# Performance work log

Hardware: AMD Instinct MI355X
Metric: run time of the kernel (lower is better)

The kernel has to match this reference:

```python
import jax, jax.numpy as jnp
import numpy as np

N_NODES = 50000
N_GRAPHS = 50
MAX_NODES = 1000  # equal-size graphs
C_IN = 128
C_OUT = 128
N_EDGES = 800000
N_LAYERS = 3
BN_EPS = 1e-5


def setup_inputs() -> dict:
    key = jax.random.key(0)
    ks = jax.random.split(key, 20)
    x = jax.random.normal(ks[0], (N_NODES, C_IN), dtype=jnp.float32)
    edge_index = jax.random.randint(ks[1], (2, N_EDGES), 0, N_NODES, dtype=jnp.int64)
    batch = jnp.repeat(jnp.arange(N_GRAPHS, dtype=jnp.int64), MAX_NODES)
    s_in = 1.0 / np.sqrt(C_IN)
    s_out = 1.0 / np.sqrt(C_OUT)
    fh_W = jax.random.normal(ks[2], (C_IN, C_OUT), dtype=jnp.float32) * s_in
    fh_b = jnp.zeros((C_OUT,), dtype=jnp.float32)
    W1 = jax.random.normal(ks[3], (N_LAYERS, C_OUT, C_OUT), dtype=jnp.float32) * s_out
    b1 = jnp.zeros((N_LAYERS, C_OUT), dtype=jnp.float32)
    g1 = jnp.ones((N_LAYERS, C_OUT), dtype=jnp.float32)
    be1 = jnp.zeros((N_LAYERS, C_OUT), dtype=jnp.float32)
    W2 = jax.random.normal(ks[4], (N_LAYERS, C_OUT, C_OUT), dtype=jnp.float32) * s_out
    b2 = jnp.zeros((N_LAYERS, C_OUT), dtype=jnp.float32)
    g2 = jnp.ones((N_LAYERS, C_OUT), dtype=jnp.float32)
    be2 = jnp.zeros((N_LAYERS, C_OUT), dtype=jnp.float32)
    return {"x": x, "edge_index": edge_index, "batch": batch,
            "fh_W": fh_W, "fh_b": fh_b,
            "W1": W1, "b1": b1, "g1": g1, "be1": be1,
            "W2": W2, "b2": b2, "g2": g2, "be2": be2}


def _bn(h, gamma, beta):
    # training-mode BatchNorm1d over the node dim (biased variance, like torch)
    mu = jnp.mean(h, axis=0)
    var = jnp.var(h, axis=0)
    return (h - mu) * jax.lax.rsqrt(var + BN_EPS) * gamma + beta


def _mlp(h, W1, b1, g1, be1, W2, b2, g2, be2):
    h = jax.nn.relu(_bn(h @ W1 + b1, g1, be1))
    h = jax.nn.relu(_bn(h @ W2 + b2, g2, be2))
    return h


def _to_dense_batch(h, batch):
    # counts per graph -> exclusive starts -> intra-graph position
    ones = jnp.ones((h.shape[0],), dtype=jnp.int32)
    counts = jax.ops.segment_sum(ones, batch, num_segments=N_GRAPHS)
    starts = jnp.cumsum(counts) - counts
    pos = jnp.arange(h.shape[0], dtype=jnp.int32) - starts[batch]
    dense = jnp.zeros((N_GRAPHS, MAX_NODES, h.shape[1]), dtype=h.dtype)
    return dense.at[batch, pos].set(h)


def reference(x, edge_index, batch, fh_W, fh_b, W1, b1, g1, be1, W2, b2, g2, be2):
    src, dst = edge_index[0], edge_index[1]
    h = x @ fh_W + fh_b  # first_head Linear
    outs = [_to_dense_batch(h, batch)]
    for l in range(N_LAYERS):
        # GINConv: mlp((1+eps)*x + sum_{j->i} x_j), eps=0
        agg = jax.ops.segment_sum(h[src], dst, num_segments=N_NODES)
        h = _mlp(h + agg, W1[l], b1[l], g1[l], be1[l], W2[l], b2[l], g2[l], be2[l])
        outs.append(_to_dense_batch(h, batch))
    return jnp.stack(outs)  # [N_LAYERS+1, B, MAX_NODES, C]
```

## Files before the change

### kernel.cpp

```cpp
#include <hip/hip_runtime.h>

#define NN 50000
#define NE 800000
#define CC 128
#define SLAB (NN * CC)
#define BN_EPS 1e-5f

typedef __attribute__((ext_vector_type(8))) short bf16x8;
typedef __attribute__((ext_vector_type(4))) float f32x4;
typedef unsigned short ushort_t;

__device__ inline ushort_t f2bf(float v) {
  unsigned u = __builtin_bit_cast(unsigned, v);
  unsigned r = u + 0x7FFFu + ((u >> 16) & 1u);
  return (ushort_t)(r >> 16);
}

__global__ void zero_int_kernel(int* __restrict__ p, int n) {
  int i = blockIdx.x * blockDim.x + threadIdx.x;
  if (i < n) p[i] = 0;
}

__global__ void count_kernel(const int* __restrict__ dst, int* __restrict__ counts) {
  int e = blockIdx.x * blockDim.x + threadIdx.x;
  if (e < NE) atomicAdd(&counts[dst[e]], 1);
}

__global__ void scan1_kernel(const int* __restrict__ counts, int* __restrict__ excl,
                             int* __restrict__ blocksum) {
  __shared__ int s[256];
  int t = threadIdx.x;
  int i = blockIdx.x * 256 + t;
  int v = (i < NN) ? counts[i] : 0;
  s[t] = v;
  for (int off = 1; off < 256; off <<= 1) {
    __syncthreads();
    int add = (t >= off) ? s[t - off] : 0;
    __syncthreads();
    s[t] += add;
  }
  __syncthreads();
  if (i < NN) excl[i] = s[t] - v;
  if (t == 255) blocksum[blockIdx.x] = s[255];
}

__global__ void scan2_kernel(int* __restrict__ blocksum, int nb) {
  __shared__ int s[256];
  int t = threadIdx.x;
  int v = (t < nb) ? blocksum[t] : 0;
  s[t] = v;
  for (int off = 1; off < 256; off <<= 1) {
    __syncthreads();
    int add = (t >= off) ? s[t - off] : 0;
    __syncthreads();
    s[t] += add;
  }
  __syncthreads();
  if (t < nb) blocksum[t] = s[t] - v;
}

__global__ void scan3_kernel(int* __restrict__ excl, const int* __restrict__ blocksum) {
  int i = blockIdx.x * 256 + threadIdx.x;
  if (i < NN) excl[i] += blocksum[blockIdx.x];
}

__global__ void fill_kernel(const int* __restrict__ src, const int* __restrict__ dst,
                            const int* __restrict__ starts, int* __restrict__ fill,
                            int* __restrict__ bucket) {
  int e = blockIdx.x * blockDim.x + threadIdx.x;
  if (e < NE) {
    int d = dst[e];
    int pos = atomicAdd(&fill[d], 1);
    bucket[starts[d] + pos] = src[e];
  }
}

__global__ void prep_w_kernel(const float* __restrict__ fh_W, const float* __restrict__ W1,
                              const float* __restrict__ W2, short* __restrict__ whi,
                              short* __restrict__ wlo) {
  int m = blockIdx.x;
  const float* src = (m == 0) ? fh_W : ((m <= 3) ? W1 + (m - 1) * CC * CC : W2 + (m - 4) * CC * CC);
  short* hi = whi + m * CC * CC;
  short* lo = wlo + m * CC * CC;
  for (int it = 0; it < 64; ++it) {
    int idx = it * 256 + threadIdx.x;
    int j = idx & 7;
    int l = (idx >> 3) & 63;
    int nt = (idx >> 9) & 7;
    int ks = idx >> 12;
    int n = nt * 16 + (l & 15);
    int k = ks * 32 + ((l >> 4) << 3) + j;
    float v = src[k * CC + n];
    unsigned u = __builtin_bit_cast(unsigned, v);
    unsigned short h = (unsigned short)(u >> 16);
    float hf = __builtin_bit_cast(float, ((unsigned)h) << 16);
    float r = v - hf;
    unsigned ur = __builtin_bit_cast(unsigned, r);
    hi[idx] = (short)h;
    lo[idx] = (short)(ur >> 16);
  }
}

__global__ void gather_kernel(const ushort_t* __restrict__ h16, const int* __restrict__ starts,
                              const int* __restrict__ counts, const int* __restrict__ bucket,
                              float* __restrict__ agg, float* __restrict__ stats) {
  if (blockIdx.x == 0) {
    stats[threadIdx.x] = 0.f;
    stats[256 + threadIdx.x] = 0.f;
  }
  const int node = blockIdx.x * 4 + (threadIdx.x >> 6);
  const int l = threadIdx.x & 63;
  const int j16 = l & 15;
  const int q = l >> 4;
  const uint4* tbl = (const uint4*)h16;

  float acc[8];
  if (q == 0) {
    uint4 u = tbl[node * 16 + j16];
    acc[0] = __builtin_bit_cast(float, u.x << 16);
    acc[1] = __builtin_bit_cast(float, u.x & 0xFFFF0000u);
    acc[2] = __builtin_bit_cast(float, u.y << 16);
    acc[3] = __builtin_bit_cast(float, u.y & 0xFFFF0000u);
    acc[4] = __builtin_bit_cast(float, u.z << 16);
    acc[5] = __builtin_bit_cast(float, u.z & 0xFFFF0000u);
    acc[6] = __builtin_bit_cast(float, u.w << 16);
    acc[7] = __builtin_bit_cast(float, u.w & 0xFFFF0000u);
  } else {
#pragma unroll
    for (int k = 0; k < 8; ++k) acc[k] = 0.f;
  }

  const int s = starts[node];
  const int n = counts[node];
  for (int base = 0; base < n; base += 64) {
    int nb = min(n - base, 64);
    int idx = (l < nb) ? bucket[s + base + l] : 0;
    int jj = 0;
    for (; jj + 8 <= nb; jj += 8) {
      int sr0 = __shfl(idx, jj + q);
      int sr1 = __shfl(idx, jj + 4 + q);
      uint4 a = tbl[sr0 * 16 + j16];
      uint4 b = tbl[sr1 * 16 + j16];
      acc[0] += __builtin_bit_cast(float, a.x << 16);
      acc[1] += __builtin_bit_cast(float, a.x & 0xFFFF0000u);
      acc[2] += __builtin_bit_cast(float, a.y << 16);
      acc[3] += __builtin_bit_cast(float, a.y & 0xFFFF0000u);
      acc[4] += __builtin_bit_cast(float, a.z << 16);
      acc[5] += __builtin_bit_cast(float, a.z & 0xFFFF0000u);
      acc[6] += __builtin_bit_cast(float, a.w << 16);
      acc[7] += __builtin_bit_cast(float, a.w & 0xFFFF0000u);
      acc[0] += __builtin_bit_cast(float, b.x << 16);
      acc[1] += __builtin_bit_cast(float, b.x & 0xFFFF0000u);
      acc[2] += __builtin_bit_cast(float, b.y << 16);
      acc[3] += __builtin_bit_cast(float, b.y & 0xFFFF0000u);
      acc[4] += __builtin_bit_cast(float, b.z << 16);
      acc[5] += __builtin_bit_cast(float, b.z & 0xFFFF0000u);
      acc[6] += __builtin_bit_cast(float, b.w << 16);
      acc[7] += __builtin_bit_cast(float, b.w & 0xFFFF0000u);
    }
    for (; jj < nb; jj += 4) {
      int i = jj + q;
      int sr = __shfl(idx, i);
      if (i < nb) {
        uint4 a = tbl[sr * 16 + j16];
        acc[0] += __builtin_bit_cast(float, a.x << 16);
        acc[1] += __builtin_bit_cast(float, a.x & 0xFFFF0000u);
        acc[2] += __builtin_bit_cast(float, a.y << 16);
        acc[3] += __builtin_bit_cast(float, a.y & 0xFFFF0000u);
        acc[4] += __builtin_bit_cast(float, a.z << 16);
        acc[5] += __builtin_bit_cast(float, a.z & 0xFFFF0000u);
        acc[6] += __builtin_bit_cast(float, a.w << 16);
        acc[7] += __builtin_bit_cast(float, a.w & 0xFFFF0000u);
      }
    }
  }
#pragma unroll
  for (int k = 0; k < 8; ++k) {
    acc[k] += __shfl_xor(acc[k], 16);
    acc[k] += __shfl_xor(acc[k], 32);
  }
  if (q == 0) {
    float4 w0 = make_float4(acc[0], acc[1], acc[2], acc[3]);
    float4 w1 = make_float4(acc[4], acc[5], acc[6], acc[7]);
    *(float4*)&agg[node * CC + j16 * 8] = w0;
    *(float4*)&agg[node * CC + j16 * 8 + 4] = w1;
  }
}

template <bool FUSE_BN, bool STATS, bool W16>
__global__ __launch_bounds__(256) void gemm_mfma_kernel(
    const float* A, const short* __restrict__ Wp_hi, const short* __restrict__ Wp_lo,
    const float* __restrict__ bias, float* out, ushort_t* __restrict__ h16,
    const float* __restrict__ bn_a, const float* __restrict__ bn_d, float* __restrict__ stats) {
  __shared__ float As[64 * 132];
  __shared__ float sred[2 * CC];
  const int t = threadIdx.x;
  const int l = t & 63;
  const int wv = t >> 6;
  const int m0 = blockIdx.x * 64 + wv * 16;
  const int rowbase = blockIdx.x * 64;
  if (STATS) sred[t] = 0.f;

#pragma unroll
  for (int i = 0; i < 8; ++i) {
    int f = i * 256 + t;
    int r = f >> 5;
    int c = (f & 31) * 4;
    int rg = rowbase + r;
    float4 v = make_float4(0.f, 0.f, 0.f, 0.f);
    if (rg < NN) v = *(const float4*)&A[rg * CC + c];
    if (FUSE_BN) {
      v.x = fmaxf(fmaf(v.x, bn_a[c + 0], bn_d[c + 0]), 0.f);
      v.y = fmaxf(fmaf(v.y, bn_a[c + 1], bn_d[c + 1]), 0.f);
      v.z = fmaxf(fmaf(v.z, bn_a[c + 2], bn_d[c + 2]), 0.f);
      v.w = fmaxf(fmaf(v.w, bn_a[c + 3], bn_d[c + 3]), 0.f);
    }
    *(float4*)&As[r * 132 + c] = v;
  }
  __syncthreads();

  f32x4 acc[8];
#pragma unroll
  for (int i = 0; i < 8; ++i) acc[i] = (f32x4){0.f, 0.f, 0.f, 0.f};

  const int arow = (wv * 16 + (l & 15)) * 132;
  const int kg = (l >> 4) * 8;

#pragma unroll
  for (int ks = 0; ks < 4; ++ks) {
    const float* ap = &As[arow + ks * 32 + kg];
    bf16x8 ah, al;
#pragma unroll
    for (int i = 0; i < 8; ++i) {
      float a = ap[i];
      unsigned u = __builtin_bit_cast(unsigned, a);
      unsigned short hbits = (unsigned short)(u >> 16);
      float hf = __builtin_bit_cast(float, ((unsigned)hbits) << 16);
      float r = a - hf;
      unsigned ur = __builtin_bit_cast(unsigned, r);
      ah[i] = (short)hbits;
      al[i] = (short)(ur >> 16);
    }
#pragma unroll
    for (int nt = 0; nt < 8; ++nt) {
      const int base = (ks * 8 + nt) * 512 + l * 8;
      bf16x8 wh = *(const bf16x8*)&Wp_hi[base];
      bf16x8 wl = *(const bf16x8*)&Wp_lo[base];
      acc[nt] = __builtin_amdgcn_mfma_f32_16x16x32_bf16(ah, wh, acc[nt], 0, 0, 0);
      acc[nt] = __builtin_amdgcn_mfma_f32_16x16x32_bf16(al, wh, acc[nt], 0, 0, 0);
      acc[nt] = __builtin_amdgcn_mfma_f32_16x16x32_bf16(ah, wl, acc[nt], 0, 0, 0);
    }
  }

  const int rbase = m0 + (l >> 4) * 4;
  const int cn = l & 15;
#pragma unroll
  for (int nt = 0; nt < 8; ++nt) {
    int c = nt * 16 + cn;
    float bv = bias[c];
    float s = 0.f, qq = 0.f;
#pragma unroll
    for (int r = 0; r < 4; ++r) {
      int rr = rbase + r;
      if (rr < NN) {
        float v = acc[nt][r] + bv;
        out[rr * CC + c] = v;
        if (W16) h16[rr * CC + c] = f2bf(v);
        if (STATS) { s += v; qq += v * v; }
      }
    }
    if (STATS) {
      s += __shfl_xor(s, 16); s += __shfl_xor(s, 32);
      qq += __shfl_xor(qq, 16); qq += __shfl_xor(qq, 32);
      if ((l >> 4) == 0) {
        atomicAdd(&sred[c], s);
        atomicAdd(&sred[CC + c], qq);
      }
    }
  }
  if (STATS) {
    __syncthreads();
    atomicAdd(&stats[t], sred[t]);
  }
}

__global__ void finalize_kernel(const float* __restrict__ stats, const float* __restrict__ g,
                                const float* __restrict__ be, float* __restrict__ bn_a,
                                float* __restrict__ bn_d) {
  int c = threadIdx.x;
  float mu = stats[c] * (1.0f / NN);
  float var = stats[CC + c] * (1.0f / NN) - mu * mu;
  var = fmaxf(var, 0.f);
  float inv = rsqrtf(var + BN_EPS);
  float a = g[c] * inv;
  bn_a[c] = a;
  bn_d[c] = fmaf(-mu, a, be[c]);
}

__global__ void apply_kernel(const float* __restrict__ tmp, const float* __restrict__ bn_a,
                             const float* __restrict__ bn_d, float* __restrict__ outslab,
                             ushort_t* __restrict__ h16) {
  int i = blockIdx.x * blockDim.x + threadIdx.x;
  float4 v = ((const float4*)tmp)[i];
  int c = (i & 31) << 2;
  float4 a = *(const float4*)&bn_a[c];
  float4 d = *(const float4*)&bn_d[c];
  v.x = fmaxf(fmaf(v.x, a.x, d.x), 0.f);
  v.y = fmaxf(fmaf(v.y, a.y, d.y), 0.f);
  v.z = fmaxf(fmaf(v.z, a.z, d.z), 0.f);
  v.w = fmaxf(fmaf(v.w, a.w, d.w), 0.f);
  ((float4*)outslab)[i] = v;
  if (h16) {
    ushort_t p[4] = {f2bf(v.x), f2bf(v.y), f2bf(v.z), f2bf(v.w)};
    *(uint2*)&h16[i * 4] = *(uint2*)p;
  }
}

extern "C" void kernel_launch(void* const* d_in, const int* in_sizes, int n_in,
                              void* d_out, int out_size, void* d_ws, size_t ws_size,
                              hipStream_t stream) {
  const float* x    = (const float*)d_in[0];
  const int*   edge = (const int*)d_in[1];
  const float* fh_W = (const float*)d_in[3];
  const float* fh_b = (const float*)d_in[4];
  const float* W1   = (const float*)d_in[5];
  const float* b1   = (const float*)d_in[6];
  const float* g1   = (const float*)d_in[7];
  const float* be1  = (const float*)d_in[8];
  const float* W2   = (const float*)d_in[9];
  const float* b2   = (const float*)d_in[10];
  const float* g2   = (const float*)d_in[11];
  const float* be2  = (const float*)d_in[12];
  float* out = (float*)d_out;

  const int* src = edge;
  const int* dst = edge + NE;

  int* counts   = (int*)d_ws;
  int* fill     = counts + 50048;
  int* starts   = fill + 50048;
  int* blocksum = starts + 50048;
  int* bucket   = blocksum + 256;
  float* stats  = (float*)(bucket + NE);
  float* bn_a1  = stats + 512;
  float* bn_d1  = bn_a1 + CC;
  float* bn_a2  = bn_d1 + CC;
  float* bn_d2  = bn_a2 + CC;
  short* whi    = (short*)(bn_d2 + CC);
  short* wlo    = whi + 7 * CC * CC;
  ushort_t* h16 = (ushort_t*)(wlo + 7 * CC * CC);
  float* aggbuf = (float*)(h16 + SLAB);

  zero_int_kernel<<<(100096 + 255) / 256, 256, 0, stream>>>(counts, 100096);
  count_kernel<<<NE / 256, 256, 0, stream>>>(dst, counts);
  scan1_kernel<<<196, 256, 0, stream>>>(counts, starts, blocksum);
  scan2_kernel<<<1, 256, 0, stream>>>(blocksum, 196);
  scan3_kernel<<<196, 256, 0, stream>>>(starts, blocksum);
  fill_kernel<<<NE / 256, 256, 0, stream>>>(src, dst, starts, fill, bucket);

  prep_w_kernel<<<7, 256, 0, stream>>>(fh_W, W1, W2, whi, wlo);

  gemm_mfma_kernel<false, false, true><<<782, 256, 0, stream>>>(
      x, whi, wlo, fh_b, out, h16, nullptr, nullptr, nullptr);

  for (int ly = 0; ly < 3; ++ly) {
    gather_kernel<<<NN / 4, 256, 0, stream>>>(h16, starts, counts, bucket, aggbuf, stats);
    gemm_mfma_kernel<false, true, false><<<782, 256, 0, stream>>>(
        aggbuf, whi + (1 + ly) * CC * CC, wlo + (1 + ly) * CC * CC, b1 + ly * CC,
        aggbuf, nullptr, nullptr, nullptr, stats);
    finalize_kernel<<<1, 128, 0, stream>>>(stats, g1 + ly * CC, be1 + ly * CC, bn_a1, bn_d1);
    gemm_mfma_kernel<true, true, false><<<782, 256, 0, stream>>>(
        aggbuf, whi + (4 + ly) * CC * CC, wlo + (4 + ly) * CC * CC, b2 + ly * CC,
        aggbuf, nullptr, bn_a1, bn_d1, stats + 256);
    finalize_kernel<<<1, 128, 0, stream>>>(stats + 256, g2 + ly * CC, be2 + ly * CC, bn_a2, bn_d2);
    apply_kernel<<<SLAB / 4 / 256, 256, 0, stream>>>(
        aggbuf, bn_a2, bn_d2, out + (ly + 1) * SLAB, (ly < 2) ? h16 : (ushort_t*)nullptr);
  }
}
```

Measured before the change: 490.1 us.

## Store aggregation in bf16, drop LDS staging, fold BN finalize into consumers

```diff
diff --git a/kernel.cpp b/kernel.cpp
--- a/kernel.cpp
+++ b/kernel.cpp
@@ -103,7 +103,7 @@
 
 __global__ void gather_kernel(const ushort_t* __restrict__ h16, const int* __restrict__ starts,
                               const int* __restrict__ counts, const int* __restrict__ bucket,
-                              float* __restrict__ agg, float* __restrict__ stats) {
+                              ushort_t* __restrict__ agg16, float* __restrict__ stats) {
   if (blockIdx.x == 0) {
     stats[threadIdx.x] = 0.f;
     stats[256 + threadIdx.x] = 0.f;
@@ -180,78 +180,99 @@
     acc[k] += __shfl_xor(acc[k], 32);
   }
   if (q == 0) {
-    float4 w0 = make_float4(acc[0], acc[1], acc[2], acc[3]);
-    float4 w1 = make_float4(acc[4], acc[5], acc[6], acc[7]);
-    *(float4*)&agg[node * CC + j16 * 8] = w0;
-    *(float4*)&agg[node * CC + j16 * 8 + 4] = w1;
-  }
-}
-
-template <bool FUSE_BN, bool STATS, bool W16>
+    uint4 o;
+    o.x = (unsigned)f2bf(acc[0]) | ((unsigned)f2bf(acc[1]) << 16);
+    o.y = (unsigned)f2bf(acc[2]) | ((unsigned)f2bf(acc[3]) << 16);
+    o.z = (unsigned)f2bf(acc[4]) | ((unsigned)f2bf(acc[5]) << 16);
+    o.w = (unsigned)f2bf(acc[6]) | ((unsigned)f2bf(acc[7]) << 16);
+    ((uint4*)agg16)[node * 16 + j16] = o;
+  }
+}
+
+template <int MODE>
 __global__ __launch_bounds__(256) void gemm_mfma_kernel(
-    const float* A, const short* __restrict__ Wp_hi, const short* __restrict__ Wp_lo,
+    const void* Aop, const short* __restrict__ Wp_hi, const short* __restrict__ Wp_lo,
     const float* __restrict__ bias, float* out, ushort_t* __restrict__ h16,
-    const float* __restrict__ bn_a, const float* __restrict__ bn_d, float* __restrict__ stats) {
-  __shared__ float As[64 * 132];
+    const float* __restrict__ stats_in, const float* __restrict__ g,
+    const float* __restrict__ be, float* __restrict__ stats_out) {
+  constexpr bool STATS = (MODE != 0);
   __shared__ float sred[2 * CC];
   const int t = threadIdx.x;
   const int l = t & 63;
   const int wv = t >> 6;
   const int m0 = blockIdx.x * 64 + wv * 16;
-  const int rowbase = blockIdx.x * 64;
+  const int row = m0 + (l & 15);
+  const int kg = (l >> 4) * 8;
   if (STATS) sred[t] = 0.f;
 
-#pragma unroll
-  for (int i = 0; i < 8; ++i) {
-    int f = i * 256 + t;
-    int r = f >> 5;
-    int c = (f & 31) * 4;
-    int rg = rowbase + r;
-    float4 v = make_float4(0.f, 0.f, 0.f, 0.f);
-    if (rg < NN) v = *(const float4*)&A[rg * CC + c];
-    if (FUSE_BN) {
-      v.x = fmaxf(fmaf(v.x, bn_a[c + 0], bn_d[c + 0]), 0.f);
-      v.y = fmaxf(fmaf(v.y, bn_a[c + 1], bn_d[c + 1]), 0.f);
-      v.z = fmaxf(fmaf(v.z, bn_a[c + 2], bn_d[c + 2]), 0.f);
-      v.w = fmaxf(fmaf(v.w, bn_a[c + 3], bn_d[c + 3]), 0.f);
-    }
-    *(float4*)&As[r * 132 + c] = v;
-  }
-  __syncthreads();
-
   f32x4 acc[8];
 #pragma unroll
   for (int i = 0; i < 8; ++i) acc[i] = (f32x4){0.f, 0.f, 0.f, 0.f};
 
-  const int arow = (wv * 16 + (l & 15)) * 132;
-  const int kg = (l >> 4) * 8;
-
 #pragma unroll
   for (int ks = 0; ks < 4; ++ks) {
-    const float* ap = &As[arow + ks * 32 + kg];
     bf16x8 ah, al;
-#pragma unroll
-    for (int i = 0; i < 8; ++i) {
-      float a = ap[i];
-      unsigned u = __builtin_bit_cast(unsigned, a);
-      unsigned short hbits = (unsigned short)(u >> 16);
-      float hf = __builtin_bit_cast(float, ((unsigned)hbits) << 16);
-      float r = a - hf;
-      unsigned ur = __builtin_bit_cast(unsigned, r);
-      ah[i] = (short)hbits;
-      al[i] = (short)(ur >> 16);
+    if (MODE == 1) {
+      if (row < NN) {
+        ah = *(const bf16x8*)&((const ushort_t*)Aop)[row * CC + ks * 32 + kg];
+      } else {
+#pragma unroll
+        for (int i = 0; i < 8; ++i) ah[i] = 0;
+      }
+    } else {
+      float av[8];
+      if (row < NN) {
+        const float* ap = &((const float*)Aop)[row * CC + ks * 32 + kg];
+        float4 v0 = *(const float4*)ap;
+        float4 v1 = *(const float4*)(ap + 4);
+        av[0] = v0.x; av[1] = v0.y; av[2] = v0.z; av[3] = v0.w;
+        av[4] = v1.x; av[5] = v1.y; av[6] = v1.z; av[7] = v1.w;
+      } else {
+#pragma unroll
+        for (int i = 0; i < 8; ++i) av[i] = 0.f;
+      }
+      if (MODE == 2) {
+#pragma unroll
+        for (int i = 0; i < 8; ++i) {
+          int c = ks * 32 + kg + i;
+          float mu = stats_in[c] * (1.0f / NN);
+          float var = stats_in[CC + c] * (1.0f / NN) - mu * mu;
+          var = fmaxf(var, 0.f);
+          float a = g[c] * rsqrtf(var + BN_EPS);
+          float d = fmaf(-mu, a, be[c]);
+          av[i] = fmaxf(fmaf(av[i], a, d), 0.f);
+          ah[i] = (short)f2bf(av[i]);
+        }
+      } else {
+#pragma unroll
+        for (int i = 0; i < 8; ++i) {
+          unsigned u = __builtin_bit_cast(unsigned, av[i]);
+          unsigned short hbits = (unsigned short)(u >> 16);
+          float hf = __builtin_bit_cast(float, ((unsigned)hbits) << 16);
+          float r = av[i] - hf;
+          unsigned ur = __builtin_bit_cast(unsigned, r);
+          ah[i] = (short)hbits;
+          al[i] = (short)(ur >> 16);
+        }
+      }
     }
 #pragma unroll
     for (int nt = 0; nt < 8; ++nt) {
       const int base = (ks * 8 + nt) * 512 + l * 8;
       bf16x8 wh = *(const bf16x8*)&Wp_hi[base];
       bf16x8 wl = *(const bf16x8*)&Wp_lo[base];
-      acc[nt] = __builtin_amdgcn_mfma_f32_16x16x32_bf16(ah, wh, acc[nt], 0, 0, 0);
-      acc[nt] = __builtin_amdgcn_mfma_f32_16x16x32_bf16(al, wh, acc[nt], 0, 0, 0);
-      acc[nt] = __builtin_amdgcn_mfma_f32_16x16x32_bf16(ah, wl, acc[nt], 0, 0, 0);
-    }
-  }
-
+      if (MODE == 0) {
+        acc[nt] = __builtin_amdgcn_mfma_f32_16x16x32_bf16(ah, wh, acc[nt], 0, 0, 0);
+        acc[nt] = __builtin_amdgcn_mfma_f32_16x16x32_bf16(al, wh, acc[nt], 0, 0, 0);
+        acc[nt] = __builtin_amdgcn_mfma_f32_16x16x32_bf16(ah, wl, acc[nt], 0, 0, 0);
+      } else {
+        acc[nt] = __builtin_amdgcn_mfma_f32_16x16x32_bf16(ah, wh, acc[nt], 0, 0, 0);
+        acc[nt] = __builtin_amdgcn_mfma_f32_16x16x32_bf16(ah, wl, acc[nt], 0, 0, 0);
+      }
+    }
+  }
+
+  if (STATS) __syncthreads();
   const int rbase = m0 + (l >> 4) * 4;
   const int cn = l & 15;
 #pragma unroll
@@ -265,7 +286,7 @@
       if (rr < NN) {
         float v = acc[nt][r] + bv;
         out[rr * CC + c] = v;
-        if (W16) h16[rr * CC + c] = f2bf(v);
+        if (MODE == 0) h16[rr * CC + c] = f2bf(v);
         if (STATS) { s += v; qq += v * v; }
       }
     }
@@ -280,31 +301,31 @@
   }
   if (STATS) {
     __syncthreads();
-    atomicAdd(&stats[t], sred[t]);
-  }
-}
-
-__global__ void finalize_kernel(const float* __restrict__ stats, const float* __restrict__ g,
-                                const float* __restrict__ be, float* __restrict__ bn_a,
-                                float* __restrict__ bn_d) {
-  int c = threadIdx.x;
-  float mu = stats[c] * (1.0f / NN);
-  float var = stats[CC + c] * (1.0f / NN) - mu * mu;
-  var = fmaxf(var, 0.f);
-  float inv = rsqrtf(var + BN_EPS);
-  float a = g[c] * inv;
-  bn_a[c] = a;
-  bn_d[c] = fmaf(-mu, a, be[c]);
-}
-
-__global__ void apply_kernel(const float* __restrict__ tmp, const float* __restrict__ bn_a,
-                             const float* __restrict__ bn_d, float* __restrict__ outslab,
-                             ushort_t* __restrict__ h16) {
+    atomicAdd(&stats_out[t], sred[t]);
+  }
+}
+
+__global__ void apply_kernel(const float* __restrict__ tmp, const float* __restrict__ stats2,
+                             const float* __restrict__ g2, const float* __restrict__ be2,
+                             float* __restrict__ outslab, ushort_t* __restrict__ h16) {
   int i = blockIdx.x * blockDim.x + threadIdx.x;
   float4 v = ((const float4*)tmp)[i];
   int c = (i & 31) << 2;
-  float4 a = *(const float4*)&bn_a[c];
-  float4 d = *(const float4*)&bn_d[c];
+  float4 sm = *(const float4*)&stats2[c];
+  float4 sq = *(const float4*)&stats2[CC + c];
+  float4 gg = *(const float4*)&g2[c];
+  float4 bb = *(const float4*)&be2[c];
+  float4 a, d;
+  {
+    float mu = sm.x * (1.0f / NN), var = fmaxf(sq.x * (1.0f / NN) - mu * mu, 0.f);
+    a.x = gg.x * rsqrtf(var + BN_EPS); d.x = fmaf(-mu, a.x, bb.x);
+    mu = sm.y * (1.0f / NN); var = fmaxf(sq.y * (1.0f / NN) - mu * mu, 0.f);
+    a.y = gg.y * rsqrtf(var + BN_EPS); d.y = fmaf(-mu, a.y, bb.y);
+    mu = sm.z * (1.0f / NN); var = fmaxf(sq.z * (1.0f / NN) - mu * mu, 0.f);
+    a.z = gg.z * rsqrtf(var + BN_EPS); d.z = fmaf(-mu, a.z, bb.z);
+    mu = sm.w * (1.0f / NN); var = fmaxf(sq.w * (1.0f / NN) - mu * mu, 0.f);
+    a.w = gg.w * rsqrtf(var + BN_EPS); d.w = fmaf(-mu, a.w, bb.w);
+  }
   v.x = fmaxf(fmaf(v.x, a.x, d.x), 0.f);
   v.y = fmaxf(fmaf(v.y, a.y, d.y), 0.f);
   v.z = fmaxf(fmaf(v.z, a.z, d.z), 0.f);
@@ -342,14 +363,11 @@
   int* blocksum = starts + 50048;
   int* bucket   = blocksum + 256;
   float* stats  = (float*)(bucket + NE);
-  float* bn_a1  = stats + 512;
-  float* bn_d1  = bn_a1 + CC;
-  float* bn_a2  = bn_d1 + CC;
-  float* bn_d2  = bn_a2 + CC;
-  short* whi    = (short*)(bn_d2 + CC);
+  short* whi    = (short*)(stats + 512);
   short* wlo    = whi + 7 * CC * CC;
   ushort_t* h16 = (ushort_t*)(wlo + 7 * CC * CC);
-  float* aggbuf = (float*)(h16 + SLAB);
+  ushort_t* agg16 = h16 + SLAB;
+  float* tmp    = (float*)(agg16 + SLAB);
 
   zero_int_kernel<<<(100096 + 255) / 256, 256, 0, stream>>>(counts, 100096);
   count_kernel<<<NE / 256, 256, 0, stream>>>(dst, counts);
@@ -360,20 +378,19 @@
 
   prep_w_kernel<<<7, 256, 0, stream>>>(fh_W, W1, W2, whi, wlo);
 
-  gemm_mfma_kernel<false, false, true><<<782, 256, 0, stream>>>(
-      x, whi, wlo, fh_b, out, h16, nullptr, nullptr, nullptr);
+  gemm_mfma_kernel<0><<<782, 256, 0, stream>>>(
+      x, whi, wlo, fh_b, out, h16, nullptr, nullptr, nullptr, nullptr);
 
   for (int ly = 0; ly < 3; ++ly) {
-    gather_kernel<<<NN / 4, 256, 0, stream>>>(h16, starts, counts, bucket, aggbuf, stats);
-    gemm_mfma_kernel<false, true, false><<<782, 256, 0, stream>>>(
-        aggbuf, whi + (1 + ly) * CC * CC, wlo + (1 + ly) * CC * CC, b1 + ly * CC,
-        aggbuf, nullptr, nullptr, nullptr, stats);
-    finalize_kernel<<<1, 128, 0, stream>>>(stats, g1 + ly * CC, be1 + ly * CC, bn_a1, bn_d1);
-    gemm_mfma_kernel<true, true, false><<<782, 256, 0, stream>>>(
-        aggbuf, whi + (4 + ly) * CC * CC, wlo + (4 + ly) * CC * CC, b2 + ly * CC,
-        aggbuf, nullptr, bn_a1, bn_d1, stats + 256);
-    finalize_kernel<<<1, 128, 0, stream>>>(stats + 256, g2 + ly * CC, be2 + ly * CC, bn_a2, bn_d2);
+    gather_kernel<<<NN / 4, 256, 0, stream>>>(h16, starts, counts, bucket, agg16, stats);
+    gemm_mfma_kernel<1><<<782, 256, 0, stream>>>(
+        agg16, whi + (1 + ly) * CC * CC, wlo + (1 + ly) * CC * CC, b1 + ly * CC,
+        tmp, nullptr, nullptr, nullptr, nullptr, stats);
+    gemm_mfma_kernel<2><<<782, 256, 0, stream>>>(
+        tmp, whi + (4 + ly) * CC * CC, wlo + (4 + ly) * CC * CC, b2 + ly * CC,
+        tmp, nullptr, stats, g1 + ly * CC, be1 + ly * CC, stats + 256);
     apply_kernel<<<SLAB / 4 / 256, 256, 0, stream>>>(
-        aggbuf, bn_a2, bn_d2, out + (ly + 1) * SLAB, (ly < 2) ? h16 : (ushort_t*)nullptr);
-  }
-}
+        tmp, stats + 256, g2 + ly * CC, be2 + ly * CC, out + (ly + 1) * SLAB,
+        (ly < 2) ? h16 : (ushort_t*)nullptr);
+  }
+}
```

New measurement: 481.3 us. About the same (-1.8%).
